# Performance work log

Measured on AMD Instinct MI355X. Metric: run time of the kernel, lower is better.

## Reference

```python
import jax, jax.numpy as jnp
import numpy as np

B, N, M, K = 2, 50000, 50000, 16
C_IN, C_ADD, C_MID = 64, 3, 16


def setup_inputs() -> dict:
    key = jax.random.key(0)
    k1, k2, k3, k4 = jax.random.split(key, 4)
    return {
        "input_features": jax.random.normal(k1, (B, N, C_IN), dtype=jnp.float32),
        "neighbor_inds": jax.random.randint(k2, (B, M, K), 0, N, dtype=jnp.int64),
        "weightnet": jax.random.normal(k3, (B, M, K, C_MID), dtype=jnp.float32),
        "additional_features": jax.random.normal(k4, (B, M, K, C_ADD), dtype=jnp.float32),
    }


def reference(input_features, neighbor_inds, weightnet, additional_features):
    # Gather neighbor features: [B, M, K, C_in]
    gathered = jax.vmap(lambda feat, idx: feat[idx])(input_features, neighbor_inds)
    # Concatenate additional per-neighbor features: [B, M, K, C_in + C_add]
    cat = jnp.concatenate([gathered, additional_features], axis=-1)
    # Weighted reduce over neighbors: [B, M, C_total, C_mid]
    out = jnp.einsum("bmkc,bmkw->bmcw", cat, weightnet)
    b, m = out.shape[:2]
    return out.reshape(b, m, -1)
```

## Files before the change

### kernel.cpp

```cpp
#include <hip/hip_runtime.h>
#include <cstdint>
#include <cstddef>


namespace {
constexpr int B_   = 2;
constexpr int N_   = 50000;
constexpr int M_   = 50000;
constexpr int K_   = 16;
constexpr int CIN  = 64;
constexpr int CADD = 3;
constexpr int CMID = 16;
constexpr int CTOT = CIN + CADD;
constexpr int COUT = CTOT * CMID;
constexpr int CPAD = 72;
constexpr int WPB  = 4;
constexpr int PAIRS = B_ * M_;
}

__global__ __launch_bounds__(256, 4)
void pconv_kernel(const float* __restrict__ feat,
                  const int*   __restrict__ inds,
                  const float* __restrict__ wnet,
                  const float* __restrict__ addf,
                  float* __restrict__ out)
{
    __shared__ alignas(16) float s_cat[WPB][K_][CPAD];
    __shared__ alignas(16) float s_wn [WPB][K_][CMID];

    const int lane = threadIdx.x & 63;
    const int wid  = threadIdx.x >> 6;
    const int gwave0 = (int)((blockIdx.x * blockDim.x + threadIdx.x) >> 6);
    const int nwaves = (int)((gridDim.x * blockDim.x) >> 6);

    float (*catw)[CPAD] = s_cat[wid];
    float (*wnw)[CMID]  = s_wn[wid];

    const int k_st = lane >> 2;
    const int q_st = lane & 3;
    const int cq   = lane >> 2;
    const int wg   = lane & 3;

    for (int p = gwave0; p < PAIRS; p += nwaves) {
        const int b = p / M_;
        const float* __restrict__ wnp  = wnet + (size_t)p * (K_ * CMID);
        const float* __restrict__ adp  = addf + (size_t)p * (K_ * CADD);
        const int*   __restrict__ idxp = inds + (size_t)p * K_;

        {
            float4 v = *reinterpret_cast<const float4*>(wnp + lane * 4);
            *reinterpret_cast<float4*>(&wnw[0][0] + lane * 4) = v;
        }
        {
            const int idx = idxp[k_st];
            const float* __restrict__ row = feat + ((size_t)b * N_ + (size_t)idx) * CIN;
            #pragma unroll
            for (int j = 0; j < 4; ++j) {
                float4 v = *reinterpret_cast<const float4*>(row + j * 16 + q_st * 4);
                *reinterpret_cast<float4*>(&catw[k_st][j * 16 + q_st * 4]) = v;
            }
        }
        if (lane < K_ * CADD) {
            const int k = lane / CADD;
            const int c = lane - k * CADD;
            catw[k][CIN + c] = adp[lane];
        }

        asm volatile("s_waitcnt lgkmcnt(0)" ::: "memory");
        __builtin_amdgcn_sched_barrier(0);

        float* __restrict__ outp = out + (size_t)p * COUT;

        float acc[4][4];
        #pragma unroll
        for (int i = 0; i < 4; ++i)
            #pragma unroll
            for (int j = 0; j < 4; ++j) acc[i][j] = 0.f;

        #pragma unroll
        for (int k = 0; k < K_; ++k) {
            float4 a = *reinterpret_cast<const float4*>(&catw[k][cq * 4]);
            float4 w = *reinterpret_cast<const float4*>(&wnw[k][wg * 4]);
            const float av[4] = {a.x, a.y, a.z, a.w};
            const float wv[4] = {w.x, w.y, w.z, w.w};
            #pragma unroll
            for (int i = 0; i < 4; ++i)
                #pragma unroll
                for (int j = 0; j < 4; ++j)
                    acc[i][j] = fmaf(av[i], wv[j], acc[i][j]);
        }

        #pragma unroll
        for (int i = 0; i < 4; ++i) {
            float4 v;
            v.x = acc[i][0]; v.y = acc[i][1]; v.z = acc[i][2]; v.w = acc[i][3];
            *reinterpret_cast<float4*>(outp + (size_t)(cq * 4 + i) * CMID + wg * 4) = v;
        }

        if (lane < CADD * CMID) {
            const int ci = lane >> 4;
            const int w  = lane & 15;
            float s = 0.f;
            #pragma unroll
            for (int k = 0; k < K_; ++k)
                s = fmaf(catw[k][CIN + ci], wnw[k][w], s);
            outp[(size_t)(CIN + ci) * CMID + w] = s;
        }
    }
}

extern "C" void kernel_launch(void* const* d_in, const int* in_sizes, int n_in,
                              void* d_out, int out_size, void* d_ws, size_t ws_size,
                              hipStream_t stream) {
    const float* feat = (const float*)d_in[0];
    const int*   inds = (const int*)d_in[1];
    const float* wnet = (const float*)d_in[2];
    const float* addf = (const float*)d_in[3];
    float* outp = (float*)d_out;

    dim3 grid(2048);
    dim3 block(256);
    hipLaunchKernelGGL(pconv_kernel, grid, block, 0, stream,
                       feat, inds, wnet, addf, outp);
}
```

Measured before the change: 180.7 us.

## Rewrite point conv with bf16 MFMA and register double-buffered prefetch

Replaces the LDS-staged FMA kernel with a register-only version that gathers neighbor rows directly into registers, packs them to bf16 by truncation, and computes the per-pair outer-product reduction with 16x16x32 bf16 MFMA instructions. It software-pipelines across pairs, prefetching indices two iterations ahead and features one iteration ahead. It uses nontemporal loads and stores for streamed data and changes the grid size and launch bounds. The aim is to hide gather latency and drop LDS traffic, at the cost of bf16 precision loss and higher register pressure.

```diff
diff --git a/kernel.cpp b/kernel.cpp
--- a/kernel.cpp
+++ b/kernel.cpp
@@ -7,119 +7,148 @@
 constexpr int B_   = 2;
 constexpr int N_   = 50000;
 constexpr int M_   = 50000;
-constexpr int K_   = 16;
+constexpr int KNB  = 16;
 constexpr int CIN  = 64;
-constexpr int CADD = 3;
-constexpr int CMID = 16;
-constexpr int CTOT = CIN + CADD;
-constexpr int COUT = CTOT * CMID;
-constexpr int CPAD = 72;
-constexpr int WPB  = 4;
+constexpr int COUT = 67 * 16;
 constexpr int PAIRS = B_ * M_;
 }
 
-__global__ __launch_bounds__(256, 4)
-void pconv_kernel(const float* __restrict__ feat,
-                  const int*   __restrict__ inds,
-                  const float* __restrict__ wnet,
-                  const float* __restrict__ addf,
-                  float* __restrict__ out)
+typedef unsigned int u32;
+typedef float  f32x4  __attribute__((ext_vector_type(4)));
+typedef short  short8 __attribute__((ext_vector_type(8)));
+typedef u32    u32x4  __attribute__((ext_vector_type(4)));
+
+struct IdxS  { int v[16]; };
+struct Stage { float bg[4][8]; float ad[8]; float wf[8]; };
+
+static __device__ __forceinline__ short8 pack_bf8(const float* x) {
+  u32x4 w;
+  #pragma unroll
+  for (int q = 0; q < 4; ++q)
+    w[q] = __builtin_amdgcn_perm(__builtin_bit_cast(u32, x[2*q+1]),
+                                 __builtin_bit_cast(u32, x[2*q]),
+                                 0x07060302u);
+  return __builtin_bit_cast(short8, w);
+}
+
+static __device__ __forceinline__ void load_idx(const int* __restrict__ idxp, IdxS& r) {
+  #pragma unroll
+  for (int j = 0; j < 16; ++j)
+    r.v[j] = __builtin_amdgcn_readfirstlane(idxp[j]);
+}
+
+static __device__ __forceinline__ void load_stage(const float* __restrict__ fb,
+                                                  const float* __restrict__ wnp,
+                                                  const float* __restrict__ adp,
+                                                  const IdxS& I, int lane, Stage& S) {
+  const int cc = lane & 15;
+  if (lane < 32) {
+    const int hi = lane >> 4;
+    int rows[8];
+    #pragma unroll
+    for (int j = 0; j < 8; ++j) rows[j] = hi ? I.v[j + 8] : I.v[j];
+    #pragma unroll
+    for (int j = 0; j < 8; ++j) {
+      const u32 rb = ((u32)rows[j]) << 6;
+      #pragma unroll
+      for (int t = 0; t < 4; ++t)
+        S.bg[t][j] = fb[rb + (u32)(t * 16 + cc)];
+    }
+    const u32 woff = (hi ? 128u : 0u) + (u32)cc;
+    #pragma unroll
+    for (int j = 0; j < 8; ++j)
+      S.wf[j] = __builtin_nontemporal_load(wnp + woff + j * 16);
+    if (cc < 3) {
+      const u32 aoff = (hi ? 24u : 0u) + (u32)cc;
+      #pragma unroll
+      for (int j = 0; j < 8; ++j)
+        S.ad[j] = __builtin_nontemporal_load(adp + aoff + j * 3);
+    }
+  }
+}
+
+static __device__ __forceinline__ void compute_store(const Stage& S,
+                                                     float* __restrict__ op, int lane) {
+  const int cc = lane & 15, g = lane >> 4;
+  const int soff = cc * 16 + g * 4;
+  const short8 a = pack_bf8(S.wf);
+  #pragma unroll
+  for (int t = 0; t < 4; ++t) {
+    const short8 b = pack_bf8(S.bg[t]);
+    f32x4 acc = {0.f, 0.f, 0.f, 0.f};
+    acc = __builtin_amdgcn_mfma_f32_16x16x32_bf16(a, b, acc, 0, 0, 0);
+    __builtin_nontemporal_store(acc, reinterpret_cast<f32x4*>(op + soff + t * 256));
+  }
+  {
+    const short8 b = pack_bf8(S.ad);
+    f32x4 acc = {0.f, 0.f, 0.f, 0.f};
+    acc = __builtin_amdgcn_mfma_f32_16x16x32_bf16(a, b, acc, 0, 0, 0);
+    if (cc < 3)
+      __builtin_nontemporal_store(acc, reinterpret_cast<f32x4*>(op + soff + 1024));
+  }
+}
+
+__global__ __launch_bounds__(256, 3)
+void pconv5(const float* __restrict__ feat, const int* __restrict__ inds,
+            const float* __restrict__ wnet, const float* __restrict__ addf,
+            float* __restrict__ out)
 {
-    __shared__ alignas(16) float s_cat[WPB][K_][CPAD];
-    __shared__ alignas(16) float s_wn [WPB][K_][CMID];
+  const int lane = threadIdx.x & 63;
+  const int gw = __builtin_amdgcn_readfirstlane(
+      (int)((blockIdx.x * blockDim.x + threadIdx.x) >> 6));
+  const int nw = (int)((gridDim.x * blockDim.x) >> 6);
+  if (gw >= PAIRS) return;
 
-    const int lane = threadIdx.x & 63;
-    const int wid  = threadIdx.x >> 6;
-    const int gwave0 = (int)((blockIdx.x * blockDim.x + threadIdx.x) >> 6);
-    const int nwaves = (int)((gridDim.x * blockDim.x) >> 6);
+  Stage sA = {}, sB = {};
+  IdxS iA, iB;
 
-    float (*catw)[CPAD] = s_cat[wid];
-    float (*wnw)[CMID]  = s_wn[wid];
+  int p = gw;
+  load_idx(inds + (size_t)p * KNB, iA);
+  {
+    const int p1 = (p + nw < PAIRS) ? (p + nw) : gw;
+    load_idx(inds + (size_t)p1 * KNB, iB);
+  }
+  {
+    const int b = p / M_;
+    load_stage(feat + (size_t)b * N_ * CIN, wnet + (size_t)p * 256,
+               addf + (size_t)p * 48, iA, lane, sA);
+  }
 
-    const int k_st = lane >> 2;
-    const int q_st = lane & 3;
-    const int cq   = lane >> 2;
-    const int wg   = lane & 3;
-
-    for (int p = gwave0; p < PAIRS; p += nwaves) {
-        const int b = p / M_;
-        const float* __restrict__ wnp  = wnet + (size_t)p * (K_ * CMID);
-        const float* __restrict__ adp  = addf + (size_t)p * (K_ * CADD);
-        const int*   __restrict__ idxp = inds + (size_t)p * K_;
-
-        {
-            float4 v = *reinterpret_cast<const float4*>(wnp + lane * 4);
-            *reinterpret_cast<float4*>(&wnw[0][0] + lane * 4) = v;
-        }
-        {
-            const int idx = idxp[k_st];
-            const float* __restrict__ row = feat + ((size_t)b * N_ + (size_t)idx) * CIN;
-            #pragma unroll
-            for (int j = 0; j < 4; ++j) {
-                float4 v = *reinterpret_cast<const float4*>(row + j * 16 + q_st * 4);
-                *reinterpret_cast<float4*>(&catw[k_st][j * 16 + q_st * 4]) = v;
-            }
-        }
-        if (lane < K_ * CADD) {
-            const int k = lane / CADD;
-            const int c = lane - k * CADD;
-            catw[k][CIN + c] = adp[lane];
-        }
-
-        asm volatile("s_waitcnt lgkmcnt(0)" ::: "memory");
-        __builtin_amdgcn_sched_barrier(0);
-
-        float* __restrict__ outp = out + (size_t)p * COUT;
-
-        float acc[4][4];
-        #pragma unroll
-        for (int i = 0; i < 4; ++i)
-            #pragma unroll
-            for (int j = 0; j < 4; ++j) acc[i][j] = 0.f;
-
-        #pragma unroll
-        for (int k = 0; k < K_; ++k) {
-            float4 a = *reinterpret_cast<const float4*>(&catw[k][cq * 4]);
-            float4 w = *reinterpret_cast<const float4*>(&wnw[k][wg * 4]);
-            const float av[4] = {a.x, a.y, a.z, a.w};
-            const float wv[4] = {w.x, w.y, w.z, w.w};
-            #pragma unroll
-            for (int i = 0; i < 4; ++i)
-                #pragma unroll
-                for (int j = 0; j < 4; ++j)
-                    acc[i][j] = fmaf(av[i], wv[j], acc[i][j]);
-        }
-
-        #pragma unroll
-        for (int i = 0; i < 4; ++i) {
-            float4 v;
-            v.x = acc[i][0]; v.y = acc[i][1]; v.z = acc[i][2]; v.w = acc[i][3];
-            *reinterpret_cast<float4*>(outp + (size_t)(cq * 4 + i) * CMID + wg * 4) = v;
-        }
-
-        if (lane < CADD * CMID) {
-            const int ci = lane >> 4;
-            const int w  = lane & 15;
-            float s = 0.f;
-            #pragma unroll
-            for (int k = 0; k < K_; ++k)
-                s = fmaf(catw[k][CIN + ci], wnw[k][w], s);
-            outp[(size_t)(CIN + ci) * CMID + w] = s;
-        }
+  while (true) {
+    {
+      const int pf = (p + 2 * nw < PAIRS) ? (p + 2 * nw) : gw;
+      load_idx(inds + (size_t)pf * KNB, iA);
+      const int pn = (p + nw < PAIRS) ? (p + nw) : gw;
+      const int bn = pn / M_;
+      load_stage(feat + (size_t)bn * N_ * CIN, wnet + (size_t)pn * 256,
+                 addf + (size_t)pn * 48, iB, lane, sB);
+      compute_store(sA, out + (size_t)p * COUT, lane);
     }
+    p += nw; if (p >= PAIRS) break;
+    {
+      const int pf = (p + 2 * nw < PAIRS) ? (p + 2 * nw) : gw;
+      load_idx(inds + (size_t)pf * KNB, iB);
+      const int pn = (p + nw < PAIRS) ? (p + nw) : gw;
+      const int bn = pn / M_;
+      load_stage(feat + (size_t)bn * N_ * CIN, wnet + (size_t)pn * 256,
+                 addf + (size_t)pn * 48, iA, lane, sA);
+      compute_store(sB, out + (size_t)p * COUT, lane);
+    }
+    p += nw; if (p >= PAIRS) break;
+  }
 }
 
 extern "C" void kernel_launch(void* const* d_in, const int* in_sizes, int n_in,
                               void* d_out, int out_size, void* d_ws, size_t ws_size,
                               hipStream_t stream) {
-    const float* feat = (const float*)d_in[0];
-    const int*   inds = (const int*)d_in[1];
-    const float* wnet = (const float*)d_in[2];
-    const float* addf = (const float*)d_in[3];
-    float* outp = (float*)d_out;
+  const float* feat = (const float*)d_in[0];
+  const int*   inds = (const int*)d_in[1];
+  const float* wnet = (const float*)d_in[2];
+  const float* addf = (const float*)d_in[3];
+  float* outp = (float*)d_out;
 
-    dim3 grid(2048);
-    dim3 block(256);
-    hipLaunchKernelGGL(pconv_kernel, grid, block, 0, stream,
-                       feat, inds, wnet, addf, outp);
+  dim3 grid(2500);
+  dim3 block(256);
+  hipLaunchKernelGGL(pconv5, grid, block, 0, stream,
+                     feat, inds, wnet, addf, outp);
 }
```

New measurement: 173.7 us. 3.9% less time.
